# Kernel tuning notes

Measured on AMD Instinct MI355X. Metric: run time of the kernel, lower is better.

Reference implementation:

```python
import jax, jax.numpy as jnp
import numpy as np

N_NODES = 50000
N_EDGES = 800000
IN_CH, HID_CH, OUT_CH = 512, 256, 128


def setup_inputs() -> dict:
    key = jax.random.key(0)
    k = jax.random.split(key, 6)
    x = jax.random.normal(k[0], (N_NODES, IN_CH), dtype=jnp.float32)
    edge_index = jax.random.randint(k[1], (2, N_EDGES), 0, N_NODES, dtype=jnp.int64)
    # Glorot-ish scaled weights
    W0 = jax.random.normal(k[2], (IN_CH, HID_CH), dtype=jnp.float32) * (1.0 / np.sqrt(IN_CH))
    b0 = jnp.zeros((HID_CH,), dtype=jnp.float32)
    W1 = jax.random.normal(k[3], (HID_CH, OUT_CH), dtype=jnp.float32) * (1.0 / np.sqrt(HID_CH))
    b1 = jnp.zeros((OUT_CH,), dtype=jnp.float32)
    PW = jax.random.normal(k[4], (OUT_CH, OUT_CH), dtype=jnp.float32) * (1.0 / np.sqrt(OUT_CH))
    Pb = jnp.zeros((OUT_CH,), dtype=jnp.float32)
    return {"x": x, "edge_index": edge_index, "W0": W0, "b0": b0,
            "W1": W1, "b1": b1, "PW": PW, "Pb": Pb}


def reference(x, edge_index, W0, b0, W1, b1, PW, Pb):
    N = x.shape[0]
    # GCN normalization with added self-loops (edge_weight=None -> ones)
    loop = jnp.arange(N, dtype=edge_index.dtype)
    src = jnp.concatenate([edge_index[0], loop])  # [E+N]
    dst = jnp.concatenate([edge_index[1], loop])
    w = jnp.ones(src.shape[0], dtype=x.dtype)
    deg = jax.ops.segment_sum(w, dst, num_segments=N)  # in-degree incl. self-loop
    dinv = jnp.where(deg > 0, jax.lax.rsqrt(jnp.maximum(deg, 1e-12)), 0.0)
    norm = dinv[src] * dinv[dst]  # [E+N]

    def gcn_conv(h, W, b):
        hl = h @ W                               # [N, F_out] linear first (PyG GCNConv)
        msg = norm[:, None] * hl[src]            # gather + scale  [E+N, F_out]
        return jax.ops.segment_sum(msg, dst, num_segments=N) + b

    # eval mode: dropout is identity
    h = jax.nn.relu(gcn_conv(x, W0, b0))
    h = gcn_conv(h, W1, b1)                      # last layer: no relu
    p = h @ PW + Pb                              # PGE linear [N, OUT]
    vals = jnp.max(p, axis=0)                    # torch.max(dim=0) -> (values, indices)
    idx = jnp.argmax(p, axis=0)
    return (h, vals, idx)
```

## Files before the change

kernel.cpp:

```cpp
#include <hip/hip_runtime.h>
#include <stdint.h>

#define N_NODES 50000
#define N_EDGES 800000
#define IN_CH   512
#define HID_CH  256
#define OUT_CH  128
#define NPAD    50048
#define SLOT    96

#define NB_E   3125
#define NB2    391

#define PZ    25
#define PW0B  (PZ + 64)
#define PW1B  (PW0B + 16)
#define PPWB  (PW1B + 8)

typedef unsigned short ushort_t;
typedef __attribute__((ext_vector_type(8))) short    short8;
typedef __attribute__((ext_vector_type(4))) float    floatx4;
typedef __attribute__((ext_vector_type(4))) _Float16 half4v;
typedef __attribute__((ext_vector_type(2))) _Float16 half2v;

__device__ inline ushort_t f2bf(float x) {
    union { float f; unsigned u; } v; v.f = x;
    unsigned r = v.u + 0x7fffu + ((v.u >> 16) & 1u);
    return (ushort_t)(r >> 16);
}
__device__ inline float bf2f(ushort_t h) {
    union { unsigned u; float f; } v; v.u = ((unsigned)h) << 16;
    return v.f;
}
__device__ inline void gl_lds16(const void* g, void* l) {
    __builtin_amdgcn_global_load_lds((const __attribute__((address_space(1))) void*)g,
                                     (__attribute__((address_space(3))) void*)l, 16, 0, 0);
}

#define SWZ(r) ((((r) >> 1) & 3) << 3)

#define SYNC_PIPE(N) do {                                                    \
    asm volatile("s_waitcnt vmcnt(" #N ") lgkmcnt(0)" ::: "memory");         \
    __builtin_amdgcn_sched_barrier(0);                                       \
    __builtin_amdgcn_s_barrier();                                            \
    __builtin_amdgcn_sched_barrier(0); } while (0)

__device__ inline void conv_splitT8(const float* __restrict__ W,
                                    ushort_t* __restrict__ WhT,
                                    ushort_t* __restrict__ WlT,
                                    int K, int N, int base) {
    float4 v0 = *(const float4*)(W + base);
    float4 v1 = *(const float4*)(W + base + 4);
    float vv[8] = {v0.x, v0.y, v0.z, v0.w, v1.x, v1.y, v1.z, v1.w};
    #pragma unroll
    for (int j = 0; j < 8; ++j) {
        int g = base + j;
        int k = g / N, n = g - k * N;
        int ks = k ^ SWZ(n);
        ushort_t h = f2bf(vv[j]);
        WhT[(size_t)n * K + ks] = h;
        WlT[(size_t)n * K + ks] = f2bf(vv[j] - bf2f(h));
    }
}

__global__ __launch_bounds__(256) void k_prep(const float* __restrict__ W0,
                                              const float* __restrict__ W1,
                                              const float* __restrict__ PW,
                                              int* __restrict__ cnt,
                                              ushort_t* W0hT, ushort_t* W0lT,
                                              ushort_t* W1hT, ushort_t* W1lT,
                                              ushort_t* PWhT, ushort_t* PWlT) {
    int b = blockIdx.x, tid = threadIdx.x;
    if (b < PZ) {
        int base = b * 2048 + tid * 8;
        #pragma unroll
        for (int j = 0; j < 8; ++j)
            if (base + j < N_NODES) cnt[base + j] = 0;
    } else if (b < PW0B) {
        conv_splitT8(W0, W0hT, W0lT, IN_CH, HID_CH, (b - PZ) * 2048 + tid * 8);
    } else if (b < PW1B) {
        conv_splitT8(W1, W1hT, W1lT, HID_CH, OUT_CH, (b - PW0B) * 2048 + tid * 8);
    } else {
        conv_splitT8(PW, PWhT, PWlT, OUT_CH, OUT_CH, (b - PW1B) * 2048 + tid * 8);
    }
}

__global__ __launch_bounds__(256) void k_bucket(const int* __restrict__ esrc,
                                                const int* __restrict__ edst,
                                                int* __restrict__ cnt,
                                                int* __restrict__ slots) {
    int e = blockIdx.x * 256 + threadIdx.x;
    if (e < N_EDGES) {
        int d = edst[e];
        int c = atomicAdd(&cnt[d], 1);
        slots[(size_t)d * SLOT + c] = esrc[e];
    }
}

__global__ __launch_bounds__(256) void k_dinv(const int* __restrict__ cnt,
                                              float* __restrict__ dinv) {
    int i = blockIdx.x * 256 + threadIdx.x;
    if (i < N_NODES) dinv[i] = rsqrtf((float)cnt[i] + 1.0f);
}

__global__ __launch_bounds__(256, 2) void gemm0_x(const float* __restrict__ A,
                                                  const ushort_t* __restrict__ BhT,
                                                  const ushort_t* __restrict__ BlT,
                                                  const float* __restrict__ dinv,
                                                  _Float16* __restrict__ C,
                                                  int M, int N) {
    constexpr int KT = IN_CH;
    constexpr int NT = KT / 32;
    __shared__ ushort_t sm[2][4][128 * 32];
    const int tid  = threadIdx.x;
    const int wave = tid >> 6, lane = tid & 63;
    const int m0 = blockIdx.y * 128, n0 = blockIdx.x * 128;

    const int sr = tid >> 1, sseg = tid & 1;
    const float* gA = A + (size_t)min(m0 + sr, M - 1) * KT + sseg * 16;
    const int swa = (sr >> 1) & 3;
    const int wo0 = sr * 32 + (((sseg * 2)     ^ swa) * 8);
    const int wo1 = sr * 32 + (((sseg * 2 + 1) ^ swa) * 8);

    const int c0 = wave * 128 + lane, c1 = c0 + 64;
    const ushort_t* gbh0 = BhT + (size_t)(n0 + (c0 >> 2)) * KT + (c0 & 3) * 8;
    const ushort_t* gbh1 = BhT + (size_t)(n0 + (c1 >> 2)) * KT + (c1 & 3) * 8;
    const ushort_t* gbl0 = BlT + (size_t)(n0 + (c0 >> 2)) * KT + (c0 & 3) * 8;
    const ushort_t* gbl1 = BlT + (size_t)(n0 + (c1 >> 2)) * KT + (c1 & 3) * 8;
    const int lo0 = wave * 1024, lo1 = wave * 1024 + 512;

    float4 q0, q1, q2, q3;
    auto loadA = [&]() {
        q0 = ((const float4*)gA)[0]; q1 = ((const float4*)gA)[1];
        q2 = ((const float4*)gA)[2]; q3 = ((const float4*)gA)[3];
        gA += 32;
    };
    auto stageB = [&](int buf) {
        gl_lds16(gbh0, &sm[buf][2][lo0]); gl_lds16(gbh1, &sm[buf][2][lo1]);
        gl_lds16(gbl0, &sm[buf][3][lo0]); gl_lds16(gbl1, &sm[buf][3][lo1]);
        gbh0 += 32; gbh1 += 32; gbl0 += 32; gbl1 += 32;
    };
    auto writeA = [&](int buf) {
        float vv[16] = {q0.x, q0.y, q0.z, q0.w, q1.x, q1.y, q1.z, q1.w,
                        q2.x, q2.y, q2.z, q2.w, q3.x, q3.y, q3.z, q3.w};
        union { ushort_t u[8]; short8 v; } h0u, h1u, l0u, l1u;
        #pragma unroll
        for (int j = 0; j < 8; ++j) {
            ushort_t h = f2bf(vv[j]);
            h0u.u[j] = h; l0u.u[j] = f2bf(vv[j] - bf2f(h));
        }
        #pragma unroll
        for (int j = 0; j < 8; ++j) {
            ushort_t h = f2bf(vv[8 + j]);
            h1u.u[j] = h; l1u.u[j] = f2bf(vv[8 + j] - bf2f(h));
        }
        *(short8*)&sm[buf][0][wo0] = h0u.v; *(short8*)&sm[buf][0][wo1] = h1u.v;
        *(short8*)&sm[buf][1][wo0] = l0u.v; *(short8*)&sm[buf][1][wo1] = l1u.v;
    };

    floatx4 zero = {0.f, 0.f, 0.f, 0.f};
    floatx4 acc[4][4];
    #pragma unroll
    for (int i = 0; i < 4; ++i)
        #pragma unroll
        for (int j = 0; j < 4; ++j) acc[i][j] = zero;

    const int wm = (wave & 1) * 64, wn = (wave >> 1) * 64;
    const int fr = lane & 15, fq = lane >> 4;
    const int sx = SWZ(fr);

    loadA();
    stageB(0);
    writeA(0);
    loadA();
    asm volatile("s_waitcnt vmcnt(4) lgkmcnt(0)" ::: "memory");
    __builtin_amdgcn_sched_barrier(0);
    __builtin_amdgcn_s_barrier();
    __builtin_amdgcn_sched_barrier(0);

    #pragma unroll 2
    for (int t = 0; t < NT; ++t) {
        const int cur = t & 1, nxt = cur ^ 1;
        if (t + 1 < NT) stageB(nxt);
        short8 afh[4], afl[4], bfh[4], bfl[4];
        #pragma unroll
        for (int tt = 0; tt < 4; ++tt) {
            int ai = (wm + tt * 16 + fr) * 32 + (fq * 8 ^ sx);
            int bi = (wn + tt * 16 + fr) * 32 + (fq * 8 ^ sx);
            afh[tt] = *(const short8*)&sm[cur][0][ai];
            afl[tt] = *(const short8*)&sm[cur][1][ai];
            bfh[tt] = *(const short8*)&sm[cur][2][bi];
            bfl[tt] = *(const short8*)&sm[cur][3][bi];
        }
        if (t + 1 < NT) {
            writeA(nxt);
            __builtin_amdgcn_sched_barrier(0);
            if (t + 2 < NT) loadA();
        }
        #pragma unroll
        for (int i = 0; i < 4; ++i)
            #pragma unroll
            for (int j = 0; j < 4; ++j) {
                acc[i][j] = __builtin_amdgcn_mfma_f32_16x16x32_bf16(afh[i], bfh[j], acc[i][j], 0, 0, 0);
                acc[i][j] = __builtin_amdgcn_mfma_f32_16x16x32_bf16(afh[i], bfl[j], acc[i][j], 0, 0, 0);
                acc[i][j] = __builtin_amdgcn_mfma_f32_16x16x32_bf16(afl[i], bfh[j], acc[i][j], 0, 0, 0);
            }
        if (t + 1 < NT) {
            if (t + 2 < NT) SYNC_PIPE(4);
            else            SYNC_PIPE(0);
        }
    }
    const int colb = n0 + wn + fr;
    #pragma unroll
    for (int i = 0; i < 4; ++i) {
        int rowb = m0 + wm + i * 16 + fq * 4;
        #pragma unroll
        for (int r = 0; r < 4; ++r) {
            int row = rowb + r;
            if (row < M) {
                float dv = dinv[row];
                _Float16* cp = C + (size_t)row * N + colb;
                cp[0]  = (_Float16)(acc[i][0][r] * dv);
                cp[16] = (_Float16)(acc[i][1][r] * dv);
                cp[32] = (_Float16)(acc[i][2][r] * dv);
                cp[48] = (_Float16)(acc[i][3][r] * dv);
            }
        }
    }
}

template <int KT>
__global__ __launch_bounds__(256, 2) void gemm_bf(const ushort_t* __restrict__ Ah,
                                                  const ushort_t* __restrict__ Al,
                                                  const ushort_t* __restrict__ BhT,
                                                  const ushort_t* __restrict__ BlT,
                                                  const float* __restrict__ dinv,
                                                  _Float16* __restrict__ C,
                                                  int M, int N) {
    constexpr int NT = KT / 32;
    __shared__ ushort_t sm[2][4][128 * 32];
    const int tid  = threadIdx.x;
    const int wave = tid >> 6, lane = tid & 63;
    const int m0 = blockIdx.y * 128, n0 = blockIdx.x * 128;

    const int c0 = wave * 128 + lane, c1 = c0 + 64;
    const int ar0 = min(m0 + (c0 >> 2), M - 1), ar1 = min(m0 + (c1 >> 2), M - 1);
    const ushort_t* gah0 = Ah + (size_t)ar0 * KT + (c0 & 3) * 8;
    const ushort_t* gah1 = Ah + (size_t)ar1 * KT + (c1 & 3) * 8;
    const ushort_t* gal0 = Al + (size_t)ar0 * KT + (c0 & 3) * 8;
    const ushort_t* gal1 = Al + (size_t)ar1 * KT + (c1 & 3) * 8;
    const ushort_t* gbh0 = BhT + (size_t)(n0 + (c0 >> 2)) * KT + (c0 & 3) * 8;
    const ushort_t* gbh1 = BhT + (size_t)(n0 + (c1 >> 2)) * KT + (c1 & 3) * 8;
    const ushort_t* gbl0 = BlT + (size_t)(n0 + (c0 >> 2)) * KT + (c0 & 3) * 8;
    const ushort_t* gbl1 = BlT + (size_t)(n0 + (c1 >> 2)) * KT + (c1 & 3) * 8;
    const int lo0 = wave * 1024, lo1 = wave * 1024 + 512;

    auto stage = [&](int buf) {
        gl_lds16(gah0, &sm[buf][0][lo0]); gl_lds16(gah1, &sm[buf][0][lo1]);
        gl_lds16(gal0, &sm[buf][1][lo0]); gl_lds16(gal1, &sm[buf][1][lo1]);
        gl_lds16(gbh0, &sm[buf][2][lo0]); gl_lds16(gbh1, &sm[buf][2][lo1]);
        gl_lds16(gbl0, &sm[buf][3][lo0]); gl_lds16(gbl1, &sm[buf][3][lo1]);
        gah0 += 32; gah1 += 32; gal0 += 32; gal1 += 32;
        gbh0 += 32; gbh1 += 32; gbl0 += 32; gbl1 += 32;
    };

    floatx4 zero = {0.f, 0.f, 0.f, 0.f};
    floatx4 acc[4][4];
    #pragma unroll
    for (int i = 0; i < 4; ++i)
        #pragma unroll
        for (int j = 0; j < 4; ++j) acc[i][j] = zero;

    const int wm = (wave & 1) * 64, wn = (wave >> 1) * 64;
    const int fr = lane & 15, fq = lane >> 4;
    const int sx = SWZ(fr);

    stage(0);
    SYNC_PIPE(0);

    #pragma unroll 2
    for (int t = 0; t < NT; ++t) {
        const int cur = t & 1, nxt = cur ^ 1;
        if (t + 1 < NT) stage(nxt);
        short8 afh[4], afl[4], bfh[4], bfl[4];
        #pragma unroll
        for (int tt = 0; tt < 4; ++tt) {
            int ai = (wm + tt * 16 + fr) * 32 + (fq * 8 ^ sx);
            int bi = (wn + tt * 16 + fr) * 32 + (fq * 8 ^ sx);
            afh[tt] = *(const short8*)&sm[cur][0][ai];
            afl[tt] = *(const short8*)&sm[cur][1][ai];
            bfh[tt] = *(const short8*)&sm[cur][2][bi];
            bfl[tt] = *(const short8*)&sm[cur][3][bi];
        }
        #pragma unroll
        for (int i = 0; i < 4; ++i)
            #pragma unroll
            for (int j = 0; j < 4; ++j) {
                acc[i][j] = __builtin_amdgcn_mfma_f32_16x16x32_bf16(afh[i], bfh[j], acc[i][j], 0, 0, 0);
                acc[i][j] = __builtin_amdgcn_mfma_f32_16x16x32_bf16(afh[i], bfl[j], acc[i][j], 0, 0, 0);
                acc[i][j] = __builtin_amdgcn_mfma_f32_16x16x32_bf16(afl[i], bfh[j], acc[i][j], 0, 0, 0);
            }
        if (t + 1 < NT) SYNC_PIPE(0);
    }
    const int colb = n0 + wn + fr;
    #pragma unroll
    for (int i = 0; i < 4; ++i) {
        int rowb = m0 + wm + i * 16 + fq * 4;
        #pragma unroll
        for (int r = 0; r < 4; ++r) {
            int row = rowb + r;
            if (row < M) {
                float dv = dinv[row];
                _Float16* cp = C + (size_t)row * N + colb;
                cp[0]  = (_Float16)(acc[i][0][r] * dv);
                cp[16] = (_Float16)(acc[i][1][r] * dv);
                cp[32] = (_Float16)(acc[i][2][r] * dv);
                cp[48] = (_Float16)(acc[i][3][r] * dv);
            }
        }
    }
}

__global__ __launch_bounds__(256, 2) void gemm_pge(const ushort_t* __restrict__ Ah,
                                                   const ushort_t* __restrict__ Al,
                                                   const ushort_t* __restrict__ BhT,
                                                   const ushort_t* __restrict__ BlT,
                                                   float* __restrict__ pv,
                                                   int* __restrict__ pi,
                                                   int M) {
    constexpr int KT = OUT_CH;
    constexpr int NT = KT / 32;
    __shared__ ushort_t sm[2][4][128 * 32];
    __shared__ float redv[8][128];
    __shared__ int   redi[8][128];
    const int tid  = threadIdx.x;
    const int wave = tid >> 6, lane = tid & 63;
    const int m0 = blockIdx.x * 128;

    const int c0 = wave * 128 + lane, c1 = c0 + 64;
    const int ar0 = min(m0 + (c0 >> 2), M - 1), ar1 = min(m0 + (c1 >> 2), M - 1);
    const ushort_t* gah0 = Ah + (size_t)ar0 * KT + (c0 & 3) * 8;
    const ushort_t* gah1 = Ah + (size_t)ar1 * KT + (c1 & 3) * 8;
    const ushort_t* gal0 = Al + (size_t)ar0 * KT + (c0 & 3) * 8;
    const ushort_t* gal1 = Al + (size_t)ar1 * KT + (c1 & 3) * 8;
    const ushort_t* gbh0 = BhT + (size_t)(c0 >> 2) * KT + (c0 & 3) * 8;
    const ushort_t* gbh1 = BhT + (size_t)(c1 >> 2) * KT + (c1 & 3) * 8;
    const ushort_t* gbl0 = BlT + (size_t)(c0 >> 2) * KT + (c0 & 3) * 8;
    const ushort_t* gbl1 = BlT + (size_t)(c1 >> 2) * KT + (c1 & 3) * 8;
    const int lo0 = wave * 1024, lo1 = wave * 1024 + 512;

    auto stage = [&](int buf) {
        gl_lds16(gah0, &sm[buf][0][lo0]); gl_lds16(gah1, &sm[buf][0][lo1]);
        gl_lds16(gal0, &sm[buf][1][lo0]); gl_lds16(gal1, &sm[buf][1][lo1]);
        gl_lds16(gbh0, &sm[buf][2][lo0]); gl_lds16(gbh1, &sm[buf][2][lo1]);
        gl_lds16(gbl0, &sm[buf][3][lo0]); gl_lds16(gbl1, &sm[buf][3][lo1]);
        gah0 += 32; gah1 += 32; gal0 += 32; gal1 += 32;
        gbh0 += 32; gbh1 += 32; gbl0 += 32; gbl1 += 32;
    };

    floatx4 zero = {0.f, 0.f, 0.f, 0.f};
    floatx4 acc[4][4];
    #pragma unroll
    for (int i = 0; i < 4; ++i)
        #pragma unroll
        for (int j = 0; j < 4; ++j) acc[i][j] = zero;

    const int wm = (wave & 1) * 64, wn = (wave >> 1) * 64;
    const int fr = lane & 15, fq = lane >> 4;
    const int sx = SWZ(fr);

    stage(0);
    SYNC_PIPE(0);

    #pragma unroll 2
    for (int t = 0; t < NT; ++t) {
        const int cur = t & 1, nxt = cur ^ 1;
        if (t + 1 < NT) stage(nxt);
        short8 afh[4], afl[4], bfh[4], bfl[4];
        #pragma unroll
        for (int tt = 0; tt < 4; ++tt) {
            int ai = (wm + tt * 16 + fr) * 32 + (fq * 8 ^ sx);
            int bi = (wn + tt * 16 + fr) * 32 + (fq * 8 ^ sx);
            afh[tt] = *(const short8*)&sm[cur][0][ai];
            afl[tt] = *(const short8*)&sm[cur][1][ai];
            bfh[tt] = *(const short8*)&sm[cur][2][bi];
            bfl[tt] = *(const short8*)&sm[cur][3][bi];
        }
        #pragma unroll
        for (int i = 0; i < 4; ++i)
            #pragma unroll
            for (int j = 0; j < 4; ++j) {
                acc[i][j] = __builtin_amdgcn_mfma_f32_16x16x32_bf16(afh[i], bfh[j], acc[i][j], 0, 0, 0);
                acc[i][j] = __builtin_amdgcn_mfma_f32_16x16x32_bf16(afh[i], bfl[j], acc[i][j], 0, 0, 0);
                acc[i][j] = __builtin_amdgcn_mfma_f32_16x16x32_bf16(afl[i], bfh[j], acc[i][j], 0, 0, 0);
            }
        if (t + 1 < NT) SYNC_PIPE(0);
    }
    __syncthreads();
    const int slot = (wave & 1) * 4 + fq;
    #pragma unroll
    for (int j = 0; j < 4; ++j) {
        float bv = -3.402823466e+38f; int bidx = 0;
        #pragma unroll
        for (int i = 0; i < 4; ++i) {
            int rowb = m0 + wm + i * 16 + fq * 4;
            #pragma unroll
            for (int r = 0; r < 4; ++r) {
                int row = rowb + r;
                float v = acc[i][j][r];
                if (row < M && v > bv) { bv = v; bidx = row; }
            }
        }
        redv[slot][wn + j * 16 + fr] = bv;
        redi[slot][wn + j * 16 + fr] = bidx;
    }
    __syncthreads();
    if (tid < 128) {
        float bv = redv[0][tid]; int bidx = redi[0][tid];
        #pragma unroll
        for (int s = 1; s < 8; ++s) {
            float v = redv[s][tid]; int ix = redi[s][tid];
            if (v > bv || (v == bv && ix < bidx)) { bv = v; bidx = ix; }
        }
        pv[blockIdx.x * 128 + tid] = bv;
        pi[blockIdx.x * 128 + tid] = bidx;
    }
}

__global__ __launch_bounds__(256) void agg256_relu_bf(const _Float16* __restrict__ hl,
                                                      const float* __restrict__ dinv,
                                                      const int* __restrict__ cnt,
                                                      const int* __restrict__ slots,
                                                      const float* __restrict__ bias,
                                                      ushort_t* __restrict__ oh,
                                                      ushort_t* __restrict__ ol) {
    int d = blockIdx.x * 4 + (threadIdx.x >> 6);
    int lane = threadIdx.x & 63;
    float di = dinv[d];
    half4v v = ((const half4v*)(hl + (size_t)d * 256))[lane];
    float ax = (float)v[0], ay = (float)v[1], az = (float)v[2], aw = (float)v[3];
    const int* sl = slots + (size_t)d * SLOT;
    int n = cnt[d];
    for (int e = 0; e < n; e += 8) {
        int s[8]; float m[8]; half4v u[8];
        #pragma unroll
        for (int j = 0; j < 8; ++j) {
            bool live = (e + j) < n;
            s[j] = live ? sl[e + j] : d;
            m[j] = live ? 1.0f : 0.0f;
        }
        #pragma unroll
        for (int j = 0; j < 8; ++j) u[j] = ((const half4v*)(hl + (size_t)s[j] * 256))[lane];
        #pragma unroll
        for (int j = 0; j < 8; ++j) {
            ax += m[j] * (float)u[j][0]; ay += m[j] * (float)u[j][1];
            az += m[j] * (float)u[j][2]; aw += m[j] * (float)u[j][3];
        }
    }
    float4 b = ((const float4*)bias)[lane];
    float rx = fmaxf(fmaf(di, ax, b.x), 0.0f), ry = fmaxf(fmaf(di, ay, b.y), 0.0f);
    float rz = fmaxf(fmaf(di, az, b.z), 0.0f), rw = fmaxf(fmaf(di, aw, b.w), 0.0f);
    ushort4 hv, lv;
    hv.x = f2bf(rx); lv.x = f2bf(rx - bf2f(hv.x));
    hv.y = f2bf(ry); lv.y = f2bf(ry - bf2f(hv.y));
    hv.z = f2bf(rz); lv.z = f2bf(rz - bf2f(hv.z));
    hv.w = f2bf(rw); lv.w = f2bf(rw - bf2f(hv.w));
    int sidx = (lane * 4) ^ SWZ(d);
    *(ushort4*)&oh[(size_t)d * 256 + sidx] = hv;
    *(ushort4*)&ol[(size_t)d * 256 + sidx] = lv;
}

__global__ __launch_bounds__(256) void agg128_bias_bf(const _Float16* __restrict__ hl,
                                                      const float* __restrict__ dinv,
                                                      const int* __restrict__ cnt,
                                                      const int* __restrict__ slots,
                                                      const float* __restrict__ bias,
                                                      float* __restrict__ out,
                                                      ushort_t* __restrict__ oh,
                                                      ushort_t* __restrict__ ol) {
    int d = blockIdx.x * 4 + (threadIdx.x >> 6);
    int lane = threadIdx.x & 63;
    float di = dinv[d];
    half2v v = ((const half2v*)(hl + (size_t)d * 128))[lane];
    float ax = (float)v[0], ay = (float)v[1];
    const int* sl = slots + (size_t)d * SLOT;
    int n = cnt[d];
    for (int e = 0; e < n; e += 8) {
        int s[8]; float m[8]; half2v u[8];
        #pragma unroll
        for (int j = 0; j < 8; ++j) {
            bool live = (e + j) < n;
            s[j] = live ? sl[e + j] : d;
            m[j] = live ? 1.0f : 0.0f;
        }
        #pragma unroll
        for (int j = 0; j < 8; ++j) u[j] = ((const half2v*)(hl + (size_t)s[j] * 128))[lane];
        #pragma unroll
        for (int j = 0; j < 8; ++j) { ax += m[j] * (float)u[j][0]; ay += m[j] * (float)u[j][1]; }
    }
    float2 b = ((const float2*)bias)[lane];
    float rx = fmaf(di, ax, b.x), ry = fmaf(di, ay, b.y);
    ((float2*)(out + (size_t)d * 128))[lane] = make_float2(rx, ry);
    ushort2 hv, lv;
    hv.x = f2bf(rx); lv.x = f2bf(rx - bf2f(hv.x));
    hv.y = f2bf(ry); lv.y = f2bf(ry - bf2f(hv.y));
    int sidx = (lane * 2) ^ SWZ(d);
    *(ushort2*)&oh[(size_t)d * 128 + sidx] = hv;
    *(ushort2*)&ol[(size_t)d * 128 + sidx] = lv;
}

__global__ __launch_bounds__(256) void k_reduce2(const float* __restrict__ pv,
                                                 const int* __restrict__ pi,
                                                 const float* __restrict__ Pb,
                                                 float* __restrict__ out) {
    int c = threadIdx.x & 127, sub = threadIdx.x >> 7;
    float best = -3.402823466e+38f;
    int bi = 0;
    for (int b = sub; b < NB2; b += 2) {
        float v = pv[b * 128 + c];
        int ix = pi[b * 128 + c];
        if (v > best || (v == best && ix < bi)) { best = v; bi = ix; }
    }
    __shared__ float sv[128];
    __shared__ int   si[128];
    if (sub == 1) { sv[c] = best; si[c] = bi; }
    __syncthreads();
    if (sub == 0) {
        float v1 = sv[c]; int i1 = si[c];
        if (v1 > best || (v1 == best && i1 < bi)) { best = v1; bi = i1; }
        out[(size_t)N_NODES * OUT_CH + c]       = best + Pb[c];
        out[(size_t)N_NODES * OUT_CH + 128 + c] = (float)bi;
    }
}

extern "C" void kernel_launch(void* const* d_in, const int* in_sizes, int n_in,
                              void* d_out, int out_size, void* d_ws, size_t ws_size,
                              hipStream_t stream) {
    const float* x  = (const float*)d_in[0];
    const int*   ei = (const int*)d_in[1];
    const float* W0 = (const float*)d_in[2];
    const float* b0 = (const float*)d_in[3];
    const float* W1 = (const float*)d_in[4];
    const float* b1 = (const float*)d_in[5];
    const float* PW = (const float*)d_in[6];
    const float* Pb = (const float*)d_in[7];
    float* out = (float*)d_out;
    const int* esrc = ei;
    const int* edst = ei + N_EDGES;

    char* w = (char*)d_ws;
    size_t off = 0;
    auto alloc = [&](size_t bytes) -> void* {
        void* p = (void*)(w + off);
        off = (off + bytes + 255) & ~(size_t)255;
        return p;
    };
    int*       cnt    = (int*)alloc((size_t)N_NODES * 4);
    float*     dinv   = (float*)alloc((size_t)N_NODES * 4);
    int*       slots  = (int*)alloc((size_t)N_NODES * SLOT * 4);
    float*     pmax_v = (float*)alloc((size_t)NB2 * 128 * 4);
    int*       pmax_i = (int*)alloc((size_t)NB2 * 128 * 4);
    _Float16*  bufH   = (_Float16*)alloc((size_t)NPAD * 256 * 2);
    ushort_t*  h0h    = (ushort_t*)alloc((size_t)N_NODES * HID_CH * 2);
    ushort_t*  h0l    = (ushort_t*)alloc((size_t)N_NODES * HID_CH * 2);
    ushort_t*  h1h    = (ushort_t*)alloc((size_t)N_NODES * OUT_CH * 2);
    ushort_t*  h1l    = (ushort_t*)alloc((size_t)N_NODES * OUT_CH * 2);
    ushort_t*  W0hT   = (ushort_t*)alloc((size_t)IN_CH * HID_CH * 2);
    ushort_t*  W0lT   = (ushort_t*)alloc((size_t)IN_CH * HID_CH * 2);
    ushort_t*  W1hT   = (ushort_t*)alloc((size_t)HID_CH * OUT_CH * 2);
    ushort_t*  W1lT   = (ushort_t*)alloc((size_t)HID_CH * OUT_CH * 2);
    ushort_t*  PWhT   = (ushort_t*)alloc((size_t)OUT_CH * OUT_CH * 2);
    ushort_t*  PWlT   = (ushort_t*)alloc((size_t)OUT_CH * OUT_CH * 2);

    k_prep<<<PPWB, 256, 0, stream>>>(W0, W1, PW, cnt,
                                     W0hT, W0lT, W1hT, W1lT, PWhT, PWlT);
    k_bucket<<<NB_E, 256, 0, stream>>>(esrc, edst, cnt, slots);
    k_dinv<<<196, 256, 0, stream>>>(cnt, dinv);

    gemm0_x<<<dim3(HID_CH / 128, NB2), 256, 0, stream>>>(
        x, W0hT, W0lT, dinv, bufH, N_NODES, HID_CH);
    agg256_relu_bf<<<N_NODES / 4, 256, 0, stream>>>(bufH, dinv, cnt, slots, b0, h0h, h0l);

    gemm_bf<HID_CH><<<dim3(1, NB2), 256, 0, stream>>>(
        h0h, h0l, W1hT, W1lT, dinv, bufH, N_NODES, OUT_CH);
    agg128_bias_bf<<<N_NODES / 4, 256, 0, stream>>>(bufH, dinv, cnt, slots, b1,
                                                    out, h1h, h1l);

    gemm_pge<<<NB2, 256, 0, stream>>>(h1h, h1l, PWhT, PWlT, pmax_v, pmax_i, N_NODES);
    k_reduce2<<<1, 256, 0, stream>>>(pmax_v, pmax_i, Pb, out);

    (void)in_sizes; (void)n_in; (void)out_size; (void)ws_size;
}
```

Measured before the change: 446.6 us.

## Fuse edge bucketing into prep kernel, simplify bf16 split, shrink aggregation blocks

```diff
diff --git a/kernel.cpp b/kernel.cpp
--- a/kernel.cpp
+++ b/kernel.cpp
@@ -12,8 +12,8 @@
 #define NB_E   3125
 #define NB2    391
 
-#define PZ    25
-#define PW0B  (PZ + 64)
+#define PBKT  NB_E
+#define PW0B  (PBKT + 64)
 #define PW1B  (PW0B + 16)
 #define PPWB  (PW1B + 8)
 
@@ -63,37 +63,30 @@
     }
 }
 
-__global__ __launch_bounds__(256) void k_prep(const float* __restrict__ W0,
+__global__ __launch_bounds__(256) void k_prep(const int* __restrict__ esrc,
+                                              const int* __restrict__ edst,
+                                              const float* __restrict__ W0,
                                               const float* __restrict__ W1,
                                               const float* __restrict__ PW,
                                               int* __restrict__ cnt,
+                                              int* __restrict__ slots,
                                               ushort_t* W0hT, ushort_t* W0lT,
                                               ushort_t* W1hT, ushort_t* W1lT,
                                               ushort_t* PWhT, ushort_t* PWlT) {
     int b = blockIdx.x, tid = threadIdx.x;
-    if (b < PZ) {
-        int base = b * 2048 + tid * 8;
-        #pragma unroll
-        for (int j = 0; j < 8; ++j)
-            if (base + j < N_NODES) cnt[base + j] = 0;
+    if (b < PBKT) {
+        int e = b * 256 + tid;
+        if (e < N_EDGES) {
+            int d = edst[e];
+            int c = atomicAdd(&cnt[d], 1);
+            slots[(size_t)d * SLOT + c] = esrc[e];
+        }
     } else if (b < PW0B) {
-        conv_splitT8(W0, W0hT, W0lT, IN_CH, HID_CH, (b - PZ) * 2048 + tid * 8);
+        conv_splitT8(W0, W0hT, W0lT, IN_CH, HID_CH, (b - PBKT) * 2048 + tid * 8);
     } else if (b < PW1B) {
         conv_splitT8(W1, W1hT, W1lT, HID_CH, OUT_CH, (b - PW0B) * 2048 + tid * 8);
     } else {
         conv_splitT8(PW, PWhT, PWlT, OUT_CH, OUT_CH, (b - PW1B) * 2048 + tid * 8);
-    }
-}
-
-__global__ __launch_bounds__(256) void k_bucket(const int* __restrict__ esrc,
-                                                const int* __restrict__ edst,
-                                                int* __restrict__ cnt,
-                                                int* __restrict__ slots) {
-    int e = blockIdx.x * 256 + threadIdx.x;
-    if (e < N_EDGES) {
-        int d = edst[e];
-        int c = atomicAdd(&cnt[d], 1);
-        slots[(size_t)d * SLOT + c] = esrc[e];
     }
 }
 
@@ -140,22 +133,24 @@
         gl_lds16(gbl0, &sm[buf][3][lo0]); gl_lds16(gbl1, &sm[buf][3][lo1]);
         gbh0 += 32; gbh1 += 32; gbl0 += 32; gbl1 += 32;
     };
+    auto splitpack = [](float a, float b, unsigned& hp, unsigned& lp) {
+        unsigned ua = __float_as_uint(a), ub = __float_as_uint(b);
+        unsigned hb = ub & 0xffff0000u;
+        float ra = a - __uint_as_float(ua & 0xffff0000u);
+        float rb = b - __uint_as_float(hb);
+        hp = (ua >> 16) | hb;
+        lp = (__float_as_uint(ra) >> 16) | (__float_as_uint(rb) & 0xffff0000u);
+    };
     auto writeA = [&](int buf) {
         float vv[16] = {q0.x, q0.y, q0.z, q0.w, q1.x, q1.y, q1.z, q1.w,
                         q2.x, q2.y, q2.z, q2.w, q3.x, q3.y, q3.z, q3.w};
-        union { ushort_t u[8]; short8 v; } h0u, h1u, l0u, l1u;
-        #pragma unroll
-        for (int j = 0; j < 8; ++j) {
-            ushort_t h = f2bf(vv[j]);
-            h0u.u[j] = h; l0u.u[j] = f2bf(vv[j] - bf2f(h));
-        }
-        #pragma unroll
-        for (int j = 0; j < 8; ++j) {
-            ushort_t h = f2bf(vv[8 + j]);
-            h1u.u[j] = h; l1u.u[j] = f2bf(vv[8 + j] - bf2f(h));
-        }
-        *(short8*)&sm[buf][0][wo0] = h0u.v; *(short8*)&sm[buf][0][wo1] = h1u.v;
-        *(short8*)&sm[buf][1][wo0] = l0u.v; *(short8*)&sm[buf][1][wo1] = l1u.v;
+        unsigned hp[8], lp[8];
+        #pragma unroll
+        for (int j = 0; j < 8; ++j) splitpack(vv[2 * j], vv[2 * j + 1], hp[j], lp[j]);
+        *(uint4*)&sm[buf][0][wo0] = make_uint4(hp[0], hp[1], hp[2], hp[3]);
+        *(uint4*)&sm[buf][0][wo1] = make_uint4(hp[4], hp[5], hp[6], hp[7]);
+        *(uint4*)&sm[buf][1][wo0] = make_uint4(lp[0], lp[1], lp[2], lp[3]);
+        *(uint4*)&sm[buf][1][wo1] = make_uint4(lp[4], lp[5], lp[6], lp[7]);
     };
 
     floatx4 zero = {0.f, 0.f, 0.f, 0.f};
@@ -427,14 +422,14 @@
     }
 }
 
-__global__ __launch_bounds__(256) void agg256_relu_bf(const _Float16* __restrict__ hl,
+__global__ __launch_bounds__(128) void agg256_relu_bf(const _Float16* __restrict__ hl,
                                                       const float* __restrict__ dinv,
                                                       const int* __restrict__ cnt,
                                                       const int* __restrict__ slots,
                                                       const float* __restrict__ bias,
                                                       ushort_t* __restrict__ oh,
                                                       ushort_t* __restrict__ ol) {
-    int d = blockIdx.x * 4 + (threadIdx.x >> 6);
+    int d = blockIdx.x * 2 + (threadIdx.x >> 6);
     int lane = threadIdx.x & 63;
     float di = dinv[d];
     half4v v = ((const half4v*)(hl + (size_t)d * 256))[lane];
@@ -470,7 +465,7 @@
     *(ushort4*)&ol[(size_t)d * 256 + sidx] = lv;
 }
 
-__global__ __launch_bounds__(256) void agg128_bias_bf(const _Float16* __restrict__ hl,
+__global__ __launch_bounds__(128) void agg128_bias_bf(const _Float16* __restrict__ hl,
                                                       const float* __restrict__ dinv,
                                                       const int* __restrict__ cnt,
                                                       const int* __restrict__ slots,
@@ -478,7 +473,7 @@
                                                       float* __restrict__ out,
                                                       ushort_t* __restrict__ oh,
                                                       ushort_t* __restrict__ ol) {
-    int d = blockIdx.x * 4 + (threadIdx.x >> 6);
+    int d = blockIdx.x * 2 + (threadIdx.x >> 6);
     int lane = threadIdx.x & 63;
     float di = dinv[d];
     half2v v = ((const half2v*)(hl + (size_t)d * 128))[lane];
@@ -572,18 +567,18 @@
     ushort_t*  PWhT   = (ushort_t*)alloc((size_t)OUT_CH * OUT_CH * 2);
     ushort_t*  PWlT   = (ushort_t*)alloc((size_t)OUT_CH * OUT_CH * 2);
 
-    k_prep<<<PPWB, 256, 0, stream>>>(W0, W1, PW, cnt,
+    hipMemsetAsync(cnt, 0, (size_t)N_NODES * 4, stream);
+    k_prep<<<PPWB, 256, 0, stream>>>(esrc, edst, W0, W1, PW, cnt, slots,
                                      W0hT, W0lT, W1hT, W1lT, PWhT, PWlT);
-    k_bucket<<<NB_E, 256, 0, stream>>>(esrc, edst, cnt, slots);
     k_dinv<<<196, 256, 0, stream>>>(cnt, dinv);
 
     gemm0_x<<<dim3(HID_CH / 128, NB2), 256, 0, stream>>>(
         x, W0hT, W0lT, dinv, bufH, N_NODES, HID_CH);
-    agg256_relu_bf<<<N_NODES / 4, 256, 0, stream>>>(bufH, dinv, cnt, slots, b0, h0h, h0l);
+    agg256_relu_bf<<<N_NODES / 2, 128, 0, stream>>>(bufH, dinv, cnt, slots, b0, h0h, h0l);
 
     gemm_bf<HID_CH><<<dim3(1, NB2), 256, 0, stream>>>(
         h0h, h0l, W1hT, W1lT, dinv, bufH, N_NODES, OUT_CH);
-    agg128_bias_bf<<<N_NODES / 4, 256, 0, stream>>>(bufH, dinv, cnt, slots, b1,
+    agg128_bias_bf<<<N_NODES / 2, 128, 0, stream>>>(bufH, dinv, cnt, slots, b1,
                                                     out, h1h, h1l);
 
     gemm_pge<<<NB2, 256, 0, stream>>>(h1h, h1l, PWhT, PWlT, pmax_v, pmax_i, N_NODES);
```

Measured after the change: 461.5 us. 3.3% more time.
